# Kernel optimization log

Measured on AMD Instinct MI355X. Metric: run time of the kernel, lower is better.

Reference implementation:

```python
import jax, jax.numpy as jnp
import numpy as np

N = 50000          # nodes
E = 1_600_000      # edges (avg degree 32)
IN = 128           # in_channels
H1, C1 = 4, 8      # conv1: heads=4, out=8 -> concat 32
OUT = 64           # out_channels (conv2, heads=1)
NEG_SLOPE = 0.2    # PyG GATConv default LeakyReLU slope


def _gat_layer(x, edge_index, W, att_src, att_dst, bias, heads, out_ch):
    """PyG-style GATConv (concat=True, add_self_loops=True).
    x: [N, F_in], edge_index: [2, E], W: [F_in, heads*out_ch],
    att_src/att_dst: [heads, out_ch], bias: [heads*out_ch].
    """
    n = x.shape[0]
    loops = jnp.arange(n)
    src = jnp.concatenate([edge_index[0], loops])  # message source j
    dst = jnp.concatenate([edge_index[1], loops])  # aggregation target i

    h = (x @ W).reshape(n, heads, out_ch)                 # [N, H, C]
    a_src = jnp.sum(h * att_src, axis=-1)                 # [N, H]
    a_dst = jnp.sum(h * att_dst, axis=-1)                 # [N, H]

    logits = jax.nn.leaky_relu(a_src[src] + a_dst[dst], NEG_SLOPE)  # [E', H]
    # segment softmax over incoming edges of each destination node
    m = jax.ops.segment_max(logits, dst, num_segments=n)            # [N, H]
    e = jnp.exp(logits - m[dst])
    s = jax.ops.segment_sum(e, dst, num_segments=n)                 # [N, H]
    alpha = e / (s[dst] + 1e-16)                                    # [E', H]

    msg = h[src] * alpha[..., None]                                 # [E', H, C]
    out = jax.ops.segment_sum(msg, dst, num_segments=n)             # [N, H, C]
    return out.reshape(n, heads * out_ch) + bias


def setup_inputs() -> dict:
    key = jax.random.key(0)
    ks = jax.random.split(key, 10)
    g = 0.1
    x = jax.random.normal(ks[0], (N, IN), jnp.float32)
    edge_index = jax.random.randint(ks[1], (2, E), 0, N, dtype=jnp.int64)
    W1 = jax.random.normal(ks[2], (IN, H1 * C1), jnp.float32) * g
    att_src1 = jax.random.normal(ks[3], (H1, C1), jnp.float32) * g
    att_dst1 = jax.random.normal(ks[4], (H1, C1), jnp.float32) * g
    b1 = jnp.zeros((H1 * C1,), jnp.float32)
    W2 = jax.random.normal(ks[5], (H1 * C1, OUT), jnp.float32) * g
    att_src2 = jax.random.normal(ks[6], (1, OUT), jnp.float32) * g
    att_dst2 = jax.random.normal(ks[7], (1, OUT), jnp.float32) * g
    b2 = jnp.zeros((OUT,), jnp.float32)
    return {"x": x, "edge_index": edge_index,
            "W1": W1, "att_src1": att_src1, "att_dst1": att_dst1, "b1": b1,
            "W2": W2, "att_src2": att_src2, "att_dst2": att_dst2, "b2": b2}


def reference(x, edge_index, W1, att_src1, att_dst1, b1, W2, att_src2, att_dst2, b2):
    h = _gat_layer(x, edge_index, W1, att_src1, att_dst1, b1, H1, C1)   # [N, 32]
    h = jax.nn.relu(h)
    out = _gat_layer(h, edge_index, W2, att_src2, att_dst2, b2, 1, OUT)  # [N, 64]
    return out
```

## Files before the change

kernel.cpp:

```cpp
#include <hip/hip_runtime.h>
#include <hip/hip_bf16.h>

#define IN_CH 128
#define H1C1  32
#define NH1   4
#define OUTC  64
#define NEG   0.2f
#define RPAD  8
#define BSH   6
#define BSZ   64
#define NBMAX 1024
#define CHUNK 4096
#define CAP   3072
#define PCAP  3584

typedef __hip_bfloat16 bf16;
typedef unsigned int u32;
typedef unsigned short u16;

__device__ __forceinline__ u16 f2bf_bits(float f) {
  bf16 v = __float2bfloat16(f);
  return *(u16*)&v;
}
__device__ __forceinline__ float bflo(u32 g) { return __uint_as_float(g << 16); }
__device__ __forceinline__ float bfhi(u32 g) { return __uint_as_float(g & 0xFFFF0000u); }


__global__ __launch_bounds__(256) void k_bin(
    const int* __restrict__ ei, int* __restrict__ bucket_fill,
    u32* __restrict__ data, int E, int n, int nb) {
  __shared__ int cnt[NBMAX];
  __shared__ int lbase[NBMAX];
  __shared__ int gbase[NBMAX];
  __shared__ u32 staged[CHUNK];
  int t = threadIdx.x;
  int lane = t & 63, wid = t >> 6;
  for (int b = t; b < nb; b += 256) cnt[b] = 0;
  __syncthreads();
  long base = (long)blockIdx.x * CHUNK;
  long totE = (long)E + n;
  u32 pk[CHUNK / 256];
  int bk[CHUNK / 256];
#pragma unroll
  for (int i = 0; i < CHUNK / 256; i++) {
    long e = base + i * 256 + t;
    if (e < totE) {
      int j, d;
      if (e < E) {
        j = ei[e]; d = ei[E + e];
        j = j < 0 ? 0 : (j >= n ? n - 1 : j);
        d = d < 0 ? 0 : (d >= n ? n - 1 : d);
      } else { j = d = (int)(e - E); }
      bk[i] = d >> BSH;
      pk[i] = ((u32)d << 16) | (u32)j;
      atomicAdd(&cnt[bk[i]], 1);
    } else bk[i] = -1;
  }
  __syncthreads();
  if (wid == 0) {
    int carry = 0;
    for (int b0 = 0; b0 < nb; b0 += 64) {
      int i = b0 + lane;
      int v = (i < nb) ? cnt[i] : 0;
      int orig = v;
      for (int off = 1; off < 64; off <<= 1) {
        int u = __shfl_up(v, off, 64);
        if (lane >= off) v += u;
      }
      if (i < nb) lbase[i] = carry + v - orig;
      carry += __shfl(v, 63, 64);
    }
  }
  __syncthreads();
  for (int b = t; b < nb; b += 256) {
    int c = cnt[b];
    gbase[b] = c ? atomicAdd(&bucket_fill[b], c) : 0;
    cnt[b] = 0;
  }
  __syncthreads();
#pragma unroll
  for (int i = 0; i < CHUNK / 256; i++) {
    if (bk[i] >= 0) {
      int loc = atomicAdd(&cnt[bk[i]], 1);
      staged[lbase[bk[i]] + loc] = pk[i];
    }
  }
  __syncthreads();
  long remL = totE - base;
  int rem = remL > CHUNK ? CHUNK : (int)remL;
  for (int idx = t; idx < rem; idx += 256) {
    u32 p = staged[idx];
    int b = (int)(p >> 16) >> BSH;
    int off2 = gbase[b] + (idx - lbase[b]);
    if (off2 < CAP) data[(size_t)b * CAP + off2] = p;
  }
}

__global__ __launch_bounds__(256) void k_bucket_scatter(
    const u32* __restrict__ data, const int* __restrict__ bucket_fill,
    int2* __restrict__ rowse, int* __restrict__ col, int n) {
  __shared__ int cur[BSZ];
  __shared__ int rp[BSZ];
  __shared__ int pd[BSZ];
  int t = threadIdx.x;
  int b = blockIdx.x;
  if (t < BSZ) cur[t] = 0;
  __syncthreads();
  int s = b * CAP;
  int cnt = bucket_fill[b];
  if (cnt > CAP) cnt = CAP;
  for (int i = t; i < cnt; i += 256)
    atomicAdd(&cur[(data[s + i] >> 16) & (BSZ - 1)], 1);
  __syncthreads();
  if (t < 64) {
    int raw = cur[t];
    int v = (raw + RPAD - 1) & ~(RPAD - 1);
    int orig = v;
    for (int off = 1; off < 64; off <<= 1) {
      int u = __shfl_up(v, off, 64);
      if (t >= off) v += u;
    }
    int r = b * PCAP + v - orig;
    rp[t] = r;
    pd[t] = orig;
    cur[t] = r;
    int node = (b << BSH) + t;
    if (node < n) rowse[node] = make_int2(r, r + orig);
  }
  __syncthreads();
  for (int i = t; i < cnt; i += 256) {
    u32 p = data[s + i];
    int dl = (int)(p >> 16) & (BSZ - 1);
    int pos = atomicAdd(&cur[dl], 1);
    col[pos] = (int)(p & 0xFFFFu);
  }
  __syncthreads();
  if (t < 64) {
    int c = cur[t];
    int end = rp[t] + pd[t];
    for (int k = c; k < end; k++) col[k] = n;
  }
}

__global__ __launch_bounds__(256) void k_l1_transform(
    const float* __restrict__ x, const float* __restrict__ W1,
    const float* __restrict__ as1, const float* __restrict__ ad1,
    u16* __restrict__ h1b, float* __restrict__ a_src, float* __restrict__ a_dst,
    int n) {
  __shared__ float W1s[32 * 128];
  __shared__ float xs[8 * IN_CH];
  int t = threadIdx.x;
  for (int idx = t; idx < IN_CH * H1C1; idx += 256) {
    int k = idx >> 5, m = idx & 31;
    W1s[(k >> 2) * 128 + m * 4 + (k & 3)] = W1[idx];
  }
  int base = blockIdx.x * 8;
  for (int idx = t; idx < 8 * IN_CH; idx += 256) {
    int row = idx >> 7, k = idx & 127;
    int nb = base + row;
    xs[idx] = (nb < n) ? x[(size_t)nb * IN_CH + k] : 0.f;
  }
  __syncthreads();
  int nl = t >> 5, m = t & 31;
  int node = base + nl;
  float acc = 0.f;
#pragma unroll
  for (int kg = 0; kg < 32; kg++) {
    float4 xv = *(const float4*)(xs + nl * IN_CH + kg * 4);
    float4 wv = *(const float4*)(W1s + kg * 128 + m * 4);
    acc += xv.x * wv.x + xv.y * wv.y + xv.z * wv.z + xv.w * wv.w;
  }
  float vs = acc * as1[m];
  float vd = acc * ad1[m];
  for (int off = 1; off < 8; off <<= 1) {
    vs += __shfl_xor(vs, off, 64);
    vd += __shfl_xor(vd, off, 64);
  }
  if (node < n) {
    h1b[node * H1C1 + m] = f2bf_bits(acc);
    if ((m & 7) == 0) {
      a_src[node * NH1 + (m >> 3)] = vs;
      a_dst[node * NH1 + (m >> 3)] = vd;
    }
  }
  if (blockIdx.x == 0) {
    if (t < H1C1) h1b[n * H1C1 + t] = 0;
    if (t < NH1)  a_src[n * NH1 + t] = -1e30f;
  }
}

__global__ __launch_bounds__(256) void k_l1_agg(
    const int2* __restrict__ rowse, const int* __restrict__ col,
    const u16* __restrict__ h1b, const float* __restrict__ a_src,
    const float* __restrict__ a_dst, const float* __restrict__ b1,
    const float* __restrict__ W2, const float* __restrict__ as2,
    const float* __restrict__ ad2,
    u16* __restrict__ h2, float* __restrict__ a_src2, float* __restrict__ a_dst2,
    int n) {
  __shared__ float W2s[8 * 256];
  __shared__ float hsh[4][H1C1];
  __shared__ float wsh[4][64][NH1];
  int t = threadIdx.x;
  int wid = t >> 6, lane = t & 63;
  for (int idx = t; idx < H1C1 * OUTC; idx += 256) {
    int k = idx >> 6, c = idx & 63;
    W2s[(k >> 2) * 256 + c * 4 + (k & 3)] = W2[idx];
  }
  int node = blockIdx.x * 4 + wid;
  int o = lane >> 3, u = lane & 7;
  int hd = u >> 1;
  if (node < n) {
    int2 se = rowse[node];
    int rs = se.x, re = se.y;
    float4 ad = *(const float4*)(a_dst + node * NH1);
    float a0 = 0.f, a1 = 0.f, a2 = 0.f, a3 = 0.f, sw = 0.f;
    for (int tb = rs; tb < re; tb += 64) {
      int kmax = re - tb; if (kmax > 64) kmax = 64;
      int jreg = 0;
      if (lane < kmax) {
        jreg = col[tb + lane];
        float4 as = *(const float4*)(a_src + jreg * NH1);
        float l0 = as.x + ad.x; l0 = l0 > 0.f ? l0 : NEG * l0;
        float l1 = as.y + ad.y; l1 = l1 > 0.f ? l1 : NEG * l1;
        float l2 = as.z + ad.z; l2 = l2 > 0.f ? l2 : NEG * l2;
        float l3 = as.w + ad.w; l3 = l3 > 0.f ? l3 : NEG * l3;
        float4 wv;
        wv.x = __expf(l0); wv.y = __expf(l1);
        wv.z = __expf(l2); wv.w = __expf(l3);
        *(float4*)(&wsh[wid][lane][0]) = wv;
      }
      for (int k = 0; k < kmax; k += 8) {
        int j = __shfl(jreg, k + o, 64);
        float wgt = wsh[wid][k + o][hd];
        uint2 g = *(const uint2*)(h1b + j * H1C1 + 4 * u);
        a0 += wgt * bflo(g.x);
        a1 += wgt * bfhi(g.x);
        a2 += wgt * bflo(g.y);
        a3 += wgt * bfhi(g.y);
        sw += wgt;
      }
    }
    for (int off = 8; off < 64; off <<= 1) {
      a0 += __shfl_xor(a0, off, 64);
      a1 += __shfl_xor(a1, off, 64);
      a2 += __shfl_xor(a2, off, 64);
      a3 += __shfl_xor(a3, off, 64);
      sw += __shfl_xor(sw, off, 64);
    }
    if (o == 0) {
      float inv = 1.f / (sw + 1e-16f);
      int c = 4 * u;
      hsh[wid][c]     = fmaxf(a0 * inv + b1[c], 0.f);
      hsh[wid][c + 1] = fmaxf(a1 * inv + b1[c + 1], 0.f);
      hsh[wid][c + 2] = fmaxf(a2 * inv + b1[c + 2], 0.f);
      hsh[wid][c + 3] = fmaxf(a3 * inv + b1[c + 3], 0.f);
    }
  }
  __syncthreads();
  float acc = 0.f;
#pragma unroll
  for (int kg = 0; kg < 8; kg++) {
    float4 hv = *(const float4*)(&hsh[wid][kg * 4]);
    float4 wv = *(const float4*)(W2s + kg * 256 + lane * 4);
    acc += hv.x * wv.x + hv.y * wv.y + hv.z * wv.z + hv.w * wv.w;
  }
  float vs = acc * as2[lane];
  float vd = acc * ad2[lane];
  for (int off = 1; off < 64; off <<= 1) {
    vs += __shfl_xor(vs, off, 64);
    vd += __shfl_xor(vd, off, 64);
  }
  if (node < n) {
    h2[node * OUTC + lane] = f2bf_bits(acc);
    if (lane == 0) { a_src2[node] = vs; a_dst2[node] = vd; }
  }
  if (blockIdx.x == 0) {
    if (t < OUTC) h2[n * OUTC + t] = 0;
    if (t == 0)   a_src2[n] = -1e30f;
  }
}

__global__ __launch_bounds__(256) void k_l2_agg(
    const int2* __restrict__ rowse, const int* __restrict__ col,
    const u16* __restrict__ h2, const float* __restrict__ a_src2,
    const float* __restrict__ a_dst2, const float* __restrict__ b2v,
    float* __restrict__ out, int n) {
  __shared__ float wsh[4][64];
  int t = threadIdx.x;
  int wid = t >> 6, lane = t & 63;
  int node = blockIdx.x * 4 + wid;
  if (node >= n) return;
  int o = lane >> 4, u = lane & 15;
  int2 se = rowse[node];
  int rs = se.x, re = se.y;
  float ad = a_dst2[node];
  float a0 = 0.f, a1 = 0.f, a2 = 0.f, a3 = 0.f, sw = 0.f;
  for (int tb = rs; tb < re; tb += 64) {
    int kmax = re - tb; if (kmax > 64) kmax = 64;
    int jreg = 0;
    if (lane < kmax) {
      jreg = col[tb + lane];
      float lg = a_src2[jreg] + ad;
      lg = lg > 0.f ? lg : NEG * lg;
      wsh[wid][lane] = __expf(lg);
    }
    for (int k = 0; k < kmax; k += 4) {
      int j = __shfl(jreg, k + o, 64);
      float wgt = wsh[wid][k + o];
      uint2 g = *(const uint2*)(h2 + j * OUTC + 4 * u);
      a0 += wgt * bflo(g.x);
      a1 += wgt * bfhi(g.x);
      a2 += wgt * bflo(g.y);
      a3 += wgt * bfhi(g.y);
      sw += wgt;
    }
  }
  for (int off = 16; off < 64; off <<= 1) {
    a0 += __shfl_xor(a0, off, 64);
    a1 += __shfl_xor(a1, off, 64);
    a2 += __shfl_xor(a2, off, 64);
    a3 += __shfl_xor(a3, off, 64);
    sw += __shfl_xor(sw, off, 64);
  }
  if (o == 0) {
    float inv = 1.f / (sw + 1e-16f);
    int c = 4 * u;
    float4 ov;
    ov.x = a0 * inv + b2v[c];
    ov.y = a1 * inv + b2v[c + 1];
    ov.z = a2 * inv + b2v[c + 2];
    ov.w = a3 * inv + b2v[c + 3];
    *(float4*)(out + node * OUTC + c) = ov;
  }
}


extern "C" void kernel_launch(void* const* d_in, const int* in_sizes, int n_in,
                              void* d_out, int out_size, void* d_ws, size_t ws_size,
                              hipStream_t stream) {
  const float* x   = (const float*)d_in[0];
  const int*   ei  = (const int*)d_in[1];
  const float* W1  = (const float*)d_in[2];
  const float* as1 = (const float*)d_in[3];
  const float* ad1 = (const float*)d_in[4];
  const float* b1  = (const float*)d_in[5];
  const float* W2  = (const float*)d_in[6];
  const float* as2 = (const float*)d_in[7];
  const float* ad2 = (const float*)d_in[8];
  const float* b2  = (const float*)d_in[9];
  float* out = (float*)d_out;

  int n = in_sizes[0] / IN_CH;
  int E = in_sizes[1] / 2;
  int nb = (n + BSZ - 1) >> BSH;
  long tot = (long)E + n;
  int nA = (int)((tot + CHUNK - 1) / CHUNK);

  char* w = (char*)d_ws;
  auto al = [](size_t v) { return (v + 255) & ~(size_t)255; };
  size_t off = 0;
  int*  bucket_fill = (int*)(w + off);  off += al((size_t)nb * 4);
  int2* rowse       = (int2*)(w + off); off += al((size_t)(n + 1) * 8);
  u32*  data        = (u32*)(w + off);  off += al((size_t)nb * CAP * 4);
  int*  col         = (int*)(w + off);  off += al((size_t)nb * PCAP * 4);
  u16*  h1b         = (u16*)(w + off);  off += al((size_t)(n + 1) * H1C1 * 2);
  float* a_src1     = (float*)(w + off); off += al((size_t)(n + 1) * NH1 * 4);
  float* a_dst1     = (float*)(w + off); off += al((size_t)(n + 1) * NH1 * 4);
  u16*  h2          = (u16*)(w + off);  off += al((size_t)(n + 1) * OUTC * 2);
  float* a_src2     = (float*)(w + off); off += al((size_t)(n + 1) * 4);
  float* a_dst2     = (float*)(w + off); off += al((size_t)(n + 1) * 4);

  hipMemsetAsync(bucket_fill, 0, (size_t)nb * 4, stream);
  hipLaunchKernelGGL(k_bin, dim3(nA), dim3(256), 0, stream,
                     ei, bucket_fill, data, E, n, nb);
  hipLaunchKernelGGL(k_bucket_scatter, dim3(nb), dim3(256), 0, stream,
                     data, bucket_fill, rowse, col, n);

  hipLaunchKernelGGL(k_l1_transform, dim3((n + 7) / 8), dim3(256), 0, stream,
                     x, W1, as1, ad1, h1b, a_src1, a_dst1, n);
  hipLaunchKernelGGL(k_l1_agg, dim3((n + 3) / 4), dim3(256), 0, stream,
                     rowse, col, h1b, a_src1, a_dst1, b1,
                     W2, as2, ad2, h2, a_src2, a_dst2, n);

  hipLaunchKernelGGL(k_l2_agg, dim3((n + 3) / 4), dim3(256), 0, stream,
                     rowse, col, h2, a_src2, a_dst2, b2, out, n);
}
```

Before: 235.3 us.

## Process four nodes per wave in aggregation kernels and amortize W2 staging

Each wavefront in both aggregation kernels now handles four destination nodes in sequence, so a block covers 16 nodes and the grid is four times smaller. In layer 1 this spreads the per-block W2 shared-memory staging (now coalesced float4 writes) over four times as many nodes. Neighbor indices are passed through shared memory instead of lane shuffles, and the weight array is transposed to a head-major layout with padding. In exchange there are fewer waves for latency hiding and more serial work per wave, which can worsen load imbalance when node degrees vary.

```diff
diff --git a/kernel.cpp b/kernel.cpp
--- a/kernel.cpp
+++ b/kernel.cpp
@@ -198,40 +198,51 @@
     u16* __restrict__ h2, float* __restrict__ a_src2, float* __restrict__ a_dst2,
     int n) {
   __shared__ float W2s[8 * 256];
-  __shared__ float hsh[4][H1C1];
-  __shared__ float wsh[4][64][NH1];
+  __shared__ float hsh[16][H1C1];
+  __shared__ int   js[4][64];
+  __shared__ float wsh[4][NH1][68];
   int t = threadIdx.x;
   int wid = t >> 6, lane = t & 63;
-  for (int idx = t; idx < H1C1 * OUTC; idx += 256) {
-    int k = idx >> 6, c = idx & 63;
-    W2s[(k >> 2) * 256 + c * 4 + (k & 3)] = W2[idx];
-  }
-  int node = blockIdx.x * 4 + wid;
+  {
+    int c = t & 63;
+#pragma unroll
+    for (int g = 0; g < 2; g++) {
+      int kg = (t >> 6) + 4 * g;
+      float4 v;
+      v.x = W2[(kg * 4 + 0) * OUTC + c];
+      v.y = W2[(kg * 4 + 1) * OUTC + c];
+      v.z = W2[(kg * 4 + 2) * OUTC + c];
+      v.w = W2[(kg * 4 + 3) * OUTC + c];
+      *(float4*)(W2s + kg * 256 + c * 4) = v;
+    }
+  }
   int o = lane >> 3, u = lane & 7;
   int hd = u >> 1;
-  if (node < n) {
+  for (int s = 0; s < 4; s++) {
+    int node = blockIdx.x * 16 + wid * 4 + s;
+    if (node >= n) continue;
     int2 se = rowse[node];
     int rs = se.x, re = se.y;
     float4 ad = *(const float4*)(a_dst + node * NH1);
     float a0 = 0.f, a1 = 0.f, a2 = 0.f, a3 = 0.f, sw = 0.f;
     for (int tb = rs; tb < re; tb += 64) {
       int kmax = re - tb; if (kmax > 64) kmax = 64;
-      int jreg = 0;
       if (lane < kmax) {
-        jreg = col[tb + lane];
-        float4 as = *(const float4*)(a_src + jreg * NH1);
+        int j = col[tb + lane];
+        float4 as = *(const float4*)(a_src + j * NH1);
         float l0 = as.x + ad.x; l0 = l0 > 0.f ? l0 : NEG * l0;
         float l1 = as.y + ad.y; l1 = l1 > 0.f ? l1 : NEG * l1;
         float l2 = as.z + ad.z; l2 = l2 > 0.f ? l2 : NEG * l2;
         float l3 = as.w + ad.w; l3 = l3 > 0.f ? l3 : NEG * l3;
-        float4 wv;
-        wv.x = __expf(l0); wv.y = __expf(l1);
-        wv.z = __expf(l2); wv.w = __expf(l3);
-        *(float4*)(&wsh[wid][lane][0]) = wv;
+        js[wid][lane] = j;
+        wsh[wid][0][lane] = __expf(l0);
+        wsh[wid][1][lane] = __expf(l1);
+        wsh[wid][2][lane] = __expf(l2);
+        wsh[wid][3][lane] = __expf(l3);
       }
       for (int k = 0; k < kmax; k += 8) {
-        int j = __shfl(jreg, k + o, 64);
-        float wgt = wsh[wid][k + o][hd];
+        int j = js[wid][k + o];
+        float wgt = wsh[wid][hd][k + o];
         uint2 g = *(const uint2*)(h1b + j * H1C1 + 4 * u);
         a0 += wgt * bflo(g.x);
         a1 += wgt * bfhi(g.x);
@@ -250,29 +261,34 @@
     if (o == 0) {
       float inv = 1.f / (sw + 1e-16f);
       int c = 4 * u;
-      hsh[wid][c]     = fmaxf(a0 * inv + b1[c], 0.f);
-      hsh[wid][c + 1] = fmaxf(a1 * inv + b1[c + 1], 0.f);
-      hsh[wid][c + 2] = fmaxf(a2 * inv + b1[c + 2], 0.f);
-      hsh[wid][c + 3] = fmaxf(a3 * inv + b1[c + 3], 0.f);
-    }
-  }
-  __syncthreads();
-  float acc = 0.f;
+      hsh[wid * 4 + s][c]     = fmaxf(a0 * inv + b1[c], 0.f);
+      hsh[wid * 4 + s][c + 1] = fmaxf(a1 * inv + b1[c + 1], 0.f);
+      hsh[wid * 4 + s][c + 2] = fmaxf(a2 * inv + b1[c + 2], 0.f);
+      hsh[wid * 4 + s][c + 3] = fmaxf(a3 * inv + b1[c + 3], 0.f);
+    }
+  }
+  __syncthreads();
+  float as2l = as2[lane], ad2l = ad2[lane];
+  for (int r = 0; r < 4; r++) {
+    int nl = wid * 4 + r;
+    int node = blockIdx.x * 16 + nl;
+    float acc = 0.f;
 #pragma unroll
-  for (int kg = 0; kg < 8; kg++) {
-    float4 hv = *(const float4*)(&hsh[wid][kg * 4]);
-    float4 wv = *(const float4*)(W2s + kg * 256 + lane * 4);
-    acc += hv.x * wv.x + hv.y * wv.y + hv.z * wv.z + hv.w * wv.w;
-  }
-  float vs = acc * as2[lane];
-  float vd = acc * ad2[lane];
-  for (int off = 1; off < 64; off <<= 1) {
-    vs += __shfl_xor(vs, off, 64);
-    vd += __shfl_xor(vd, off, 64);
-  }
-  if (node < n) {
-    h2[node * OUTC + lane] = f2bf_bits(acc);
-    if (lane == 0) { a_src2[node] = vs; a_dst2[node] = vd; }
+    for (int kg = 0; kg < 8; kg++) {
+      float4 hv = *(const float4*)(&hsh[nl][kg * 4]);
+      float4 wv = *(const float4*)(W2s + kg * 256 + lane * 4);
+      acc += hv.x * wv.x + hv.y * wv.y + hv.z * wv.z + hv.w * wv.w;
+    }
+    float vs = acc * as2l;
+    float vd = acc * ad2l;
+    for (int off = 1; off < 64; off <<= 1) {
+      vs += __shfl_xor(vs, off, 64);
+      vd += __shfl_xor(vd, off, 64);
+    }
+    if (node < n) {
+      h2[node * OUTC + lane] = f2bf_bits(acc);
+      if (lane == 0) { a_src2[node] = vs; a_dst2[node] = vd; }
+    }
   }
   if (blockIdx.x == 0) {
     if (t < OUTC) h2[n * OUTC + t] = 0;
@@ -285,52 +301,55 @@
     const u16* __restrict__ h2, const float* __restrict__ a_src2,
     const float* __restrict__ a_dst2, const float* __restrict__ b2v,
     float* __restrict__ out, int n) {
+  __shared__ int   js[4][64];
   __shared__ float wsh[4][64];
   int t = threadIdx.x;
   int wid = t >> 6, lane = t & 63;
-  int node = blockIdx.x * 4 + wid;
-  if (node >= n) return;
   int o = lane >> 4, u = lane & 15;
-  int2 se = rowse[node];
-  int rs = se.x, re = se.y;
-  float ad = a_dst2[node];
-  float a0 = 0.f, a1 = 0.f, a2 = 0.f, a3 = 0.f, sw = 0.f;
-  for (int tb = rs; tb < re; tb += 64) {
-    int kmax = re - tb; if (kmax > 64) kmax = 64;
-    int jreg = 0;
-    if (lane < kmax) {
-      jreg = col[tb + lane];
-      float lg = a_src2[jreg] + ad;
-      lg = lg > 0.f ? lg : NEG * lg;
-      wsh[wid][lane] = __expf(lg);
-    }
-    for (int k = 0; k < kmax; k += 4) {
-      int j = __shfl(jreg, k + o, 64);
-      float wgt = wsh[wid][k + o];
-      uint2 g = *(const uint2*)(h2 + j * OUTC + 4 * u);
-      a0 += wgt * bflo(g.x);
-      a1 += wgt * bfhi(g.x);
-      a2 += wgt * bflo(g.y);
-      a3 += wgt * bfhi(g.y);
-      sw += wgt;
-    }
-  }
-  for (int off = 16; off < 64; off <<= 1) {
-    a0 += __shfl_xor(a0, off, 64);
-    a1 += __shfl_xor(a1, off, 64);
-    a2 += __shfl_xor(a2, off, 64);
-    a3 += __shfl_xor(a3, off, 64);
-    sw += __shfl_xor(sw, off, 64);
-  }
-  if (o == 0) {
-    float inv = 1.f / (sw + 1e-16f);
-    int c = 4 * u;
-    float4 ov;
-    ov.x = a0 * inv + b2v[c];
-    ov.y = a1 * inv + b2v[c + 1];
-    ov.z = a2 * inv + b2v[c + 2];
-    ov.w = a3 * inv + b2v[c + 3];
-    *(float4*)(out + node * OUTC + c) = ov;
+  for (int s = 0; s < 4; s++) {
+    int node = blockIdx.x * 16 + wid * 4 + s;
+    if (node >= n) continue;
+    int2 se = rowse[node];
+    int rs = se.x, re = se.y;
+    float ad = a_dst2[node];
+    float a0 = 0.f, a1 = 0.f, a2 = 0.f, a3 = 0.f, sw = 0.f;
+    for (int tb = rs; tb < re; tb += 64) {
+      int kmax = re - tb; if (kmax > 64) kmax = 64;
+      if (lane < kmax) {
+        int j = col[tb + lane];
+        float lg = a_src2[j] + ad;
+        lg = lg > 0.f ? lg : NEG * lg;
+        js[wid][lane] = j;
+        wsh[wid][lane] = __expf(lg);
+      }
+      for (int k = 0; k < kmax; k += 4) {
+        int j = js[wid][k + o];
+        float wgt = wsh[wid][k + o];
+        uint2 g = *(const uint2*)(h2 + j * OUTC + 4 * u);
+        a0 += wgt * bflo(g.x);
+        a1 += wgt * bfhi(g.x);
+        a2 += wgt * bflo(g.y);
+        a3 += wgt * bfhi(g.y);
+        sw += wgt;
+      }
+    }
+    for (int off = 16; off < 64; off <<= 1) {
+      a0 += __shfl_xor(a0, off, 64);
+      a1 += __shfl_xor(a1, off, 64);
+      a2 += __shfl_xor(a2, off, 64);
+      a3 += __shfl_xor(a3, off, 64);
+      sw += __shfl_xor(sw, off, 64);
+    }
+    if (o == 0) {
+      float inv = 1.f / (sw + 1e-16f);
+      int c = 4 * u;
+      float4 ov;
+      ov.x = a0 * inv + b2v[c];
+      ov.y = a1 * inv + b2v[c + 1];
+      ov.z = a2 * inv + b2v[c + 2];
+      ov.w = a3 * inv + b2v[c + 3];
+      *(float4*)(out + node * OUTC + c) = ov;
+    }
   }
 }
 
@@ -378,10 +397,10 @@
 
   hipLaunchKernelGGL(k_l1_transform, dim3((n + 7) / 8), dim3(256), 0, stream,
                      x, W1, as1, ad1, h1b, a_src1, a_dst1, n);
-  hipLaunchKernelGGL(k_l1_agg, dim3((n + 3) / 4), dim3(256), 0, stream,
+  hipLaunchKernelGGL(k_l1_agg, dim3((n + 15) / 16), dim3(256), 0, stream,
                      rowse, col, h1b, a_src1, a_dst1, b1,
                      W2, as2, ad2, h2, a_src2, a_dst2, n);
 
-  hipLaunchKernelGGL(k_l2_agg, dim3((n + 3) / 4), dim3(256), 0, stream,
+  hipLaunchKernelGGL(k_l2_agg, dim3((n + 15) / 16), dim3(256), 0, stream,
                      rowse, col, h2, a_src2, a_dst2, b2, out, n);
 }
```

After: 236.1 us. No clear change (+0.3%).
